# Kernel optimization log

Measured on AMD Instinct MI355X. Metric: run time of the kernel, lower is better.

## Reference

```python
import jax, jax.numpy as jnp
import numpy as np

ROPE_BASE = 10000.0
NEG_INF = -1e30

def _apply_rope(x):
    # x: [B, H, T, D]; interleaved-pair RoPE (torchtune style), positions along axis -2.
    B, H, T, D = x.shape
    inv_freq = 1.0 / (ROPE_BASE ** (jnp.arange(0, D, 2, dtype=jnp.float32) / D))  # [D/2]
    ang = jnp.arange(T, dtype=jnp.float32)[:, None] * inv_freq[None, :]           # [T, D/2]
    cos, sin = jnp.cos(ang), jnp.sin(ang)
    x1, x2 = x[..., 0::2], x[..., 1::2]                                           # [B,H,T,D/2]
    rot = jnp.stack([x1 * cos - x2 * sin, x1 * sin + x2 * cos], axis=-1)          # [B,H,T,D/2,2]
    return rot.reshape(B, H, T, D).astype(x.dtype)

def setup_inputs() -> dict:
    key = jax.random.key(0)
    ks = jax.random.split(key, 5)
    B, T, C = 2, 2048, 1024
    s = 1.0 / np.sqrt(C)
    return {
        "x":  jax.random.normal(ks[0], (B, T, C), jnp.float32),
        "Wq": jax.random.normal(ks[1], (C, C), jnp.float32) * s,
        "bq": jnp.zeros((C,), jnp.float32),
        "Wk": jax.random.normal(ks[2], (C, C), jnp.float32) * s,
        "bk": jnp.zeros((C,), jnp.float32),
        "Wv": jax.random.normal(ks[3], (C, C), jnp.float32) * s,
        "bv": jnp.zeros((C,), jnp.float32),
        "Wo": jax.random.normal(ks[4], (C, C), jnp.float32) * s,
        "bo": jnp.zeros((C,), jnp.float32),
    }

def reference(x, Wq, bq, Wk, bk, Wv, bv, Wo, bo):
    B, T, C = x.shape
    H = 16
    D = C // H
    # QKV projections (torch Linear: x @ W.T + b), split heads -> [B, H, T, D]
    def proj(W, b):
        return (jnp.einsum('btc,oc->bto', x, W) + b).reshape(B, T, H, D).transpose(0, 2, 1, 3)
    q = _apply_rope(proj(Wq, bq))
    k = _apply_rope(proj(Wk, bk))
    v = proj(Wv, bv)
    # Causal scaled dot-product attention
    scale = 1.0 / jnp.sqrt(jnp.asarray(D, x.dtype))
    scores = jnp.einsum('bhqd,bhkd->bhqk', q, k) * scale                          # [B,H,T,T]
    causal = jnp.tril(jnp.ones((T, T), dtype=bool))
    scores = jnp.where(causal, scores, NEG_INF)
    probs = jax.nn.softmax(scores, axis=-1)
    y = jnp.einsum('bhqk,bhkd->bhqd', probs, v)                                   # [B,H,T,D]
    y = y.transpose(0, 2, 1, 3).reshape(B, T, C)
    # Output projection (dropout is identity in eval mode)
    return jnp.einsum('btc,oc->bto', y, Wo) + bo
```

## Files before the change

kernel.cpp:

```cpp
#include <hip/hip_runtime.h>

#define BB 2
#define TT 2048
#define CC 1024
#define HH 16
#define DD 64
#define KDIM 1024
#define MROWS (BB*TT)

typedef __attribute__((ext_vector_type(8))) short  frag_b16;
typedef __attribute__((ext_vector_type(4))) float  f32x4;
typedef __attribute__((ext_vector_type(4))) unsigned short us4;
typedef __attribute__((ext_vector_type(8))) unsigned short us8;
typedef __attribute__((ext_vector_type(4))) _Float16 f16x4;
typedef __attribute__((ext_vector_type(8))) _Float16 f16x8;

__device__ __forceinline__ unsigned short f2bf(float f) {
    unsigned int u = __builtin_bit_cast(unsigned int, f);
    u += 0x7FFFu + ((u >> 16) & 1u);
    return (unsigned short)(u >> 16);
}

__device__ __forceinline__ void gl_lds16(const void* g, void* l) {
    __builtin_amdgcn_global_load_lds(
        (const __attribute__((address_space(1))) unsigned int*)g,
        (__attribute__((address_space(3))) unsigned int*)l, 16, 0, 0);
}

__global__ __launch_bounds__(256) void cvt_all(
        const float* __restrict__ x,  const float* __restrict__ w0,
        const float* __restrict__ w1, const float* __restrict__ w2,
        const float* __restrict__ w3, unsigned short* __restrict__ dst) {
    const size_t NX = (size_t)MROWS * CC;
    const size_t NW = (size_t)CC * CC;
    size_t i = ((size_t)blockIdx.x * 256 + threadIdx.x) * 4;
    const float* src; size_t off;
    if (i < NX) { src = x; off = i; }
    else {
        size_t j = i - NX;
        int t = (int)(j >> 20);
        src = (t == 0) ? w0 : (t == 1) ? w1 : (t == 2) ? w2 : w3;
        off = j & (NW - 1);
    }
    float4 f = *reinterpret_cast<const float4*>(src + off);
    us4 o;
    o.x = f2bf(f.x); o.y = f2bf(f.y); o.z = f2bf(f.z); o.w = f2bf(f.w);
    *reinterpret_cast<us4*>(dst + i) = o;
}

__global__ __launch_bounds__(256, 3) void qkv_gemm_rope(
        const unsigned short* __restrict__ X,
        const unsigned short* __restrict__ Wq,
        const unsigned short* __restrict__ Wk,
        const unsigned short* __restrict__ Wv,
        const float* __restrict__ bq, const float* __restrict__ bk,
        const float* __restrict__ bv,
        unsigned short* __restrict__ Qo,
        unsigned short* __restrict__ Ko,
        _Float16* __restrict__ VTo)
{
    const int z = blockIdx.z;
    const unsigned short* W = (z == 0) ? Wq : (z == 1) ? Wk : Wv;
    const float* bias = (z == 0) ? bq : (z == 1) ? bk : bv;

    const int tid = threadIdx.x;
    const int wave = tid >> 6;
    const int lane = tid & 63;
    const int l16 = lane & 15;
    const int quad = lane >> 4;

    const int bx = blockIdx.x * 128;
    const int by = blockIdx.y * 128;
    const int row0 = bx + (wave >> 1) * 64;
    const int col0 = by + (wave & 1) * 64;

    __shared__ __align__(16) char smem[36864];
    unsigned short (*Xa)[32] = (unsigned short(*)[32])smem;
    unsigned short (*Wb)[32] = (unsigned short(*)[32])(smem + 8192);
    _Float16 (*Vl)[64][72] = (_Float16(*)[64][72])smem;

    f32x4 acc[4][4] = {};

    const int c0 = tid, c1 = tid + 256;
    const int r0s = c0 >> 2, o0s = (c0 & 3) * 8;
    const int r1s = c1 >> 2, o1s = (c1 & 3) * 8;

    for (int kk = 0; kk < KDIM; kk += 32) {
        gl_lds16(X + (size_t)(bx + r0s) * KDIM + kk + o0s, (unsigned short*)Xa + c0 * 8);
        gl_lds16(X + (size_t)(bx + r1s) * KDIM + kk + o1s, (unsigned short*)Xa + c1 * 8);
        gl_lds16(W + (size_t)(by + r0s) * KDIM + kk + o0s, (unsigned short*)Wb + c0 * 8);
        gl_lds16(W + (size_t)(by + r1s) * KDIM + kk + o1s, (unsigned short*)Wb + c1 * 8);
        __syncthreads();

        frag_b16 a[4], b[4];
#pragma unroll
        for (int r = 0; r < 4; ++r)
            a[r] = *reinterpret_cast<const frag_b16*>(
                &Xa[(wave >> 1) * 64 + r * 16 + l16][quad * 8]);
#pragma unroll
        for (int c = 0; c < 4; ++c)
            b[c] = *reinterpret_cast<const frag_b16*>(
                &Wb[(wave & 1) * 64 + c * 16 + l16][quad * 8]);
#pragma unroll
        for (int r = 0; r < 4; ++r)
#pragma unroll
            for (int c = 0; c < 4; ++c)
                acc[r][c] = __builtin_amdgcn_mfma_f32_16x16x32_bf16(a[r], b[c], acc[r][c], 0, 0, 0);
        __syncthreads();
    }

    if (z == 2) {
#pragma unroll
        for (int r = 0; r < 4; ++r)
#pragma unroll
            for (int c = 0; c < 4; ++c) {
                f16x4 pk;
#pragma unroll
                for (int g = 0; g < 4; ++g)
                    pk[g] = (_Float16)(acc[r][c][g] + bias[col0 + c * 16 + l16]);
                *reinterpret_cast<f16x4*>(&Vl[wave][c * 16 + l16][r * 16 + quad * 4]) = pk;
            }
        const int b_ = row0 >> 11;
        const int t_base = row0 & (TT - 1);
        const int h = col0 >> 6;
        const int dl = lane >> 3;
        const int t8 = (lane & 7) * 8;
        __builtin_amdgcn_s_waitcnt(0);
#pragma unroll
        for (int i = 0; i < 8; ++i) {
            int d = i * 8 + dl;
            f16x8 v = *reinterpret_cast<const f16x8*>(&Vl[wave][d][t8]);
            *reinterpret_cast<f16x8*>(
                &VTo[((size_t)(b_ * HH + h) * DD + d) * TT + t_base + t8]) = v;
        }
    } else {
        const float qscale = (z == 0) ? 0.125f : 1.0f;
#pragma unroll
        for (int r = 0; r < 4; ++r)
#pragma unroll
            for (int c = 0; c < 4; ++c)
#pragma unroll
                for (int g = 0; g < 4; ++g) {
                    int n = row0 + r * 16 + quad * 4 + g;
                    int o = col0 + c * 16 + l16;
                    float v = acc[r][c][g] + bias[o];
                    int b_ = n >> 11;
                    int t  = n & (TT - 1);
                    int h  = o >> 6;
                    int d  = o & (DD - 1);
                    float pv = __shfl_xor(v, 1);
                    float inv = __expf(-(float)(d & ~1) * (9.210340371976184f / (float)DD));
                    float ang = (float)t * inv;
                    float sn, cs;
                    __sincosf(ang, &sn, &cs);
                    float outv = (d & 1) ? (pv * sn + v * cs) : (v * cs - pv * sn);
                    unsigned short* dst = (z == 0) ? Qo : Ko;
                    dst[((size_t)(b_ * HH + h) * TT + t) * DD + d] = f2bf(outv * qscale);
                }
    }
}

__global__ __launch_bounds__(256, 2) void attn(
        const unsigned short* __restrict__ Q,
        const unsigned short* __restrict__ K,
        const _Float16* __restrict__ VT,
        unsigned short* __restrict__ Y)
{
    const int pair = blockIdx.x;
    const int bh = blockIdx.y;
    const int tid = threadIdx.x;
    const int w = tid >> 6;
    const int lane = tid & 63;
    const int l16 = lane & 15;
    const int quad = lane >> 4;

    const unsigned short* Qp = Q + (size_t)bh * TT * DD;
    const unsigned short* Kp = K + (size_t)bh * TT * DD;
    const _Float16* Vp = VT + (size_t)bh * DD * TT;

    __shared__ unsigned short Kl[2][64][64];
    __shared__ _Float16 Vl[2][64][64];
    __shared__ unsigned short Ylds[4][16][72];

    const int ca = tid, cb = tid + 256;
    const int ra = ca >> 3, oa = ((ca & 7) ^ (ra & 7)) * 8;
    const int rb = cb >> 3, ob = ((cb & 7) ^ (rb & 7)) * 8;
    const int sw = (l16 & 7);

    const int b_ = bh >> 4, h = bh & (HH - 1);

#pragma unroll 1
    for (int seg = 0; seg < 2; ++seg) {
        const int qblk = seg ? (31 - pair) : pair;
        const int q0 = qblk * 64;
        const int q = q0 + w * 16 + l16;

        frag_b16 bq[2];
#pragma unroll
        for (int dk = 0; dk < 2; ++dk)
            bq[dk] = *reinterpret_cast<const frag_b16*>(
                Qp + (size_t)q * DD + dk * 32 + quad * 8);

        f32x4 yacc[4] = {};
        float m = -INFINITY, l = 0.f;

        const int ntiles = qblk + 1;

        gl_lds16(Kp + (size_t)ra * DD + oa, (unsigned short*)&Kl[0][0][0] + ca * 8);
        gl_lds16(Kp + (size_t)rb * DD + ob, (unsigned short*)&Kl[0][0][0] + cb * 8);
        gl_lds16(Vp + (size_t)ra * TT + oa, (_Float16*)&Vl[0][0][0] + ca * 8);
        gl_lds16(Vp + (size_t)rb * TT + ob, (_Float16*)&Vl[0][0][0] + cb * 8);

#pragma unroll 1
        for (int it = 0; it < ntiles; ++it) {
            __syncthreads();
            const int bsel = it & 1;
            if (it + 1 < ntiles) {
                const int jn = (it + 1) * 64;
                const int bn = bsel ^ 1;
                gl_lds16(Kp + (size_t)(jn + ra) * DD + oa, (unsigned short*)&Kl[bn][0][0] + ca * 8);
                gl_lds16(Kp + (size_t)(jn + rb) * DD + ob, (unsigned short*)&Kl[bn][0][0] + cb * 8);
                gl_lds16(Vp + (size_t)ra * TT + jn + oa, (_Float16*)&Vl[bn][0][0] + ca * 8);
                gl_lds16(Vp + (size_t)rb * TT + jn + ob, (_Float16*)&Vl[bn][0][0] + cb * 8);
            }
            const int j0 = it * 64;

            f32x4 s[4];
#pragma unroll
            for (int mt = 0; mt < 4; ++mt) {
                frag_b16 ak0 = *reinterpret_cast<const frag_b16*>(
                    &Kl[bsel][mt * 16 + l16][(quad ^ sw) * 8]);
                frag_b16 ak1 = *reinterpret_cast<const frag_b16*>(
                    &Kl[bsel][mt * 16 + l16][((4 + quad) ^ sw) * 8]);
                f32x4 t = {};
                t = __builtin_amdgcn_mfma_f32_16x16x32_bf16(ak0, bq[0], t, 0, 0, 0);
                t = __builtin_amdgcn_mfma_f32_16x16x32_bf16(ak1, bq[1], t, 0, 0, 0);
                s[mt] = t;
            }

            float nm = -INFINITY;
            if (it == qblk) {
#pragma unroll
                for (int mt = 0; mt < 4; ++mt)
#pragma unroll
                    for (int g = 0; g < 4; ++g) {
                        int key = j0 + mt * 16 + quad * 4 + g;
                        float v = s[mt][g];
                        if (key > q) v = -1e30f;
                        s[mt][g] = v;
                        nm = fmaxf(nm, v);
                    }
            } else {
#pragma unroll
                for (int mt = 0; mt < 4; ++mt)
#pragma unroll
                    for (int g = 0; g < 4; ++g)
                        nm = fmaxf(nm, s[mt][g]);
            }
            nm = fmaxf(nm, __shfl_xor(nm, 16));
            nm = fmaxf(nm, __shfl_xor(nm, 32));

            float mn = fmaxf(m, nm);
            float alpha = __expf(m - mn);
            m = mn;

            float rs = 0.f;
#pragma unroll
            for (int mt = 0; mt < 4; ++mt)
#pragma unroll
                for (int g = 0; g < 4; ++g) {
                    float e = __expf(s[mt][g] - m);
                    s[mt][g] = e;
                    rs += e;
                }
            rs += __shfl_xor(rs, 16);
            rs += __shfl_xor(rs, 32);
            l = l * alpha + rs;

            f16x4 pb[4];
#pragma unroll
            for (int kt = 0; kt < 4; ++kt)
#pragma unroll
                for (int g = 0; g < 4; ++g)
                    pb[kt][g] = (_Float16)s[kt][g];

#pragma unroll
            for (int dt = 0; dt < 4; ++dt) {
                f32x4 ya = yacc[dt];
#pragma unroll
                for (int g = 0; g < 4; ++g) ya[g] *= alpha;
#pragma unroll
                for (int kt = 0; kt < 4; ++kt) {
                    int colp = (kt * 2 + (quad >> 1)) ^ sw;
                    f16x4 av = *reinterpret_cast<const f16x4*>(
                        &Vl[bsel][dt * 16 + l16][colp * 8 + (quad & 1) * 4]);
                    ya = __builtin_amdgcn_mfma_f32_16x16x16f16(av, pb[kt], ya, 0, 0, 0);
                }
                yacc[dt] = ya;
            }
        }

        __syncthreads();

        float rl = 1.f / l;
#pragma unroll
        for (int dt = 0; dt < 4; ++dt)
#pragma unroll
            for (int g = 0; g < 4; ++g)
                Ylds[w][l16][dt * 16 + quad * 4 + g] = f2bf(yacc[dt][g] * rl);

#pragma unroll
        for (int i = 0; i < 2; ++i) {
            int idx = i * 64 + lane;
            int r = idx >> 3, c8 = (idx & 7) * 8;
            us8 v = *reinterpret_cast<const us8*>(&Ylds[w][r][c8]);
            *reinterpret_cast<us8*>(
                &Y[(size_t)(b_ * TT + q0 + w * 16 + r) * CC + h * DD + c8]) = v;
        }
    }
}

__global__ __launch_bounds__(256, 2) void out_gemm(
        const unsigned short* __restrict__ Y,
        const unsigned short* __restrict__ Wo,
        const float* __restrict__ bo,
        float* __restrict__ out)
{
    const int tid = threadIdx.x;
    const int wave = tid >> 6;
    const int lane = tid & 63;
    const int l16 = lane & 15;
    const int quad = lane >> 4;

    const int bx = blockIdx.x * 128;
    const int by = blockIdx.y * 128;
    const int row0 = bx + (wave >> 1) * 64;
    const int col0 = by + (wave & 1) * 64;

    __shared__ unsigned short Xa[128][32];
    __shared__ unsigned short Wb[128][32];

    f32x4 acc[4][4] = {};

    const int c0 = tid, c1 = tid + 256;
    const int r0s = c0 >> 2, o0s = (c0 & 3) * 8;
    const int r1s = c1 >> 2, o1s = (c1 & 3) * 8;

    for (int kk = 0; kk < KDIM; kk += 32) {
        gl_lds16(Y  + (size_t)(bx + r0s) * KDIM + kk + o0s, (unsigned short*)Xa + c0 * 8);
        gl_lds16(Y  + (size_t)(bx + r1s) * KDIM + kk + o1s, (unsigned short*)Xa + c1 * 8);
        gl_lds16(Wo + (size_t)(by + r0s) * KDIM + kk + o0s, (unsigned short*)Wb + c0 * 8);
        gl_lds16(Wo + (size_t)(by + r1s) * KDIM + kk + o1s, (unsigned short*)Wb + c1 * 8);
        __syncthreads();

        frag_b16 a[4], b[4];
#pragma unroll
        for (int r = 0; r < 4; ++r)
            a[r] = *reinterpret_cast<const frag_b16*>(
                &Xa[(wave >> 1) * 64 + r * 16 + l16][quad * 8]);
#pragma unroll
        for (int c = 0; c < 4; ++c)
            b[c] = *reinterpret_cast<const frag_b16*>(
                &Wb[(wave & 1) * 64 + c * 16 + l16][quad * 8]);
#pragma unroll
        for (int r = 0; r < 4; ++r)
#pragma unroll
            for (int c = 0; c < 4; ++c)
                acc[r][c] = __builtin_amdgcn_mfma_f32_16x16x32_bf16(a[r], b[c], acc[r][c], 0, 0, 0);
        __syncthreads();
    }

#pragma unroll
    for (int r = 0; r < 4; ++r)
#pragma unroll
        for (int c = 0; c < 4; ++c)
#pragma unroll
            for (int g = 0; g < 4; ++g) {
                int n = row0 + r * 16 + quad * 4 + g;
                int o = col0 + c * 16 + l16;
                out[(size_t)n * CC + o] = acc[r][c][g] + bo[o];
            }
}

extern "C" void kernel_launch(void* const* d_in, const int* in_sizes, int n_in,
                              void* d_out, int out_size, void* d_ws, size_t ws_size,
                              hipStream_t stream) {
    const float* x  = (const float*)d_in[0];
    const float* Wq = (const float*)d_in[1];
    const float* bq = (const float*)d_in[2];
    const float* Wk = (const float*)d_in[3];
    const float* bk = (const float*)d_in[4];
    const float* Wv = (const float*)d_in[5];
    const float* bv = (const float*)d_in[6];
    const float* Wo = (const float*)d_in[7];
    const float* bo = (const float*)d_in[8];
    float* out = (float*)d_out;

    unsigned short* ws = (unsigned short*)d_ws;
    const size_t NX = (size_t)MROWS * CC;
    const size_t NW = (size_t)CC * CC;
    unsigned short* xb  = ws;
    unsigned short* wqb = xb  + NX;
    unsigned short* wkb = wqb + NW;
    unsigned short* wvb = wkb + NW;
    unsigned short* wob = wvb + NW;
    unsigned short* Qr  = wob + NW;
    unsigned short* Kr  = Qr  + NX;
    _Float16*       VTb = (_Float16*)(Kr + NX);
    unsigned short* Yb  = (unsigned short*)(VTb + NX);

    const size_t NALL = NX + 4 * NW;
    cvt_all<<<dim3((unsigned)(NALL / 1024)), 256, 0, stream>>>(x, Wq, Wk, Wv, Wo, xb);

    qkv_gemm_rope<<<dim3(MROWS / 128, CC / 128, 3), 256, 0, stream>>>(
        xb, wqb, wkb, wvb, bq, bk, bv, Qr, Kr, VTb);

    attn<<<dim3(16, BB * HH), 256, 0, stream>>>(Qr, Kr, VTb, Yb);

    out_gemm<<<dim3(MROWS / 128, CC / 128), 256, 0, stream>>>(Yb, wob, bo, out);
}
```

Measured before the change: 190.0 us.

## Widen attention key tiles, use exp2 softmax, and compute RoPE incrementally

The attention kernel now processes 128-key tiles per iteration instead of 64, which halves the number of barrier and softmax steps. It folds log2(e) into the Q scale so exp2 can be used, and remaps the 1D grid so blocks are ordered by batch-head. The QKV epilogue replaces per-element sincos with a rotation recurrence built from a few sincos calls per column. The wider tiles raise LDS use and register pressure. The V-tile swizzle only XORs with the row's low 3 bits across 16 chunks, and the recurrence slightly changes RoPE numerics.

Result: faster. 183.5 us (-3.4%).

```diff
diff --git a/kernel.cpp b/kernel.cpp
--- a/kernel.cpp
+++ b/kernel.cpp
@@ -14,6 +14,8 @@
 typedef __attribute__((ext_vector_type(8))) unsigned short us8;
 typedef __attribute__((ext_vector_type(4))) _Float16 f16x4;
 typedef __attribute__((ext_vector_type(8))) _Float16 f16x8;
+
+#define EXP2F(x) __builtin_amdgcn_exp2f(x)
 
 __device__ __forceinline__ unsigned short f2bf(float f) {
     unsigned int u = __builtin_bit_cast(unsigned int, f);
@@ -134,29 +136,40 @@
                 &VTo[((size_t)(b_ * HH + h) * DD + d) * TT + t_base + t8]) = v;
         }
     } else {
-        const float qscale = (z == 0) ? 0.125f : 1.0f;
-#pragma unroll
-        for (int r = 0; r < 4; ++r)
-#pragma unroll
-            for (int c = 0; c < 4; ++c)
+        const float qsc = (z == 0) ? 0.180336888f : 1.0f;
+        unsigned short* dst = (z == 0) ? Qo : Ko;
+        const int b_ = row0 >> 11;
+        const int tq0 = (row0 & (TT - 1)) + quad * 4;
+#pragma unroll
+        for (int c = 0; c < 4; ++c) {
+            const int o = col0 + c * 16 + l16;
+            const int h = o >> 6, d = o & (DD - 1);
+            const float inv = __expf(-(float)(d & ~1) * (9.210340371976184f / (float)DD));
+            float cs0, sn0, cs1, sn1, cs16, sn16;
+            __sincosf((float)tq0 * inv, &sn0, &cs0);
+            __sincosf(inv, &sn1, &cs1);
+            __sincosf(16.f * inv, &sn16, &cs16);
+            float cr = cs0, sr = sn0;
+#pragma unroll
+            for (int r = 0; r < 4; ++r) {
+                float cg = cr, sg = sr;
 #pragma unroll
                 for (int g = 0; g < 4; ++g) {
                     int n = row0 + r * 16 + quad * 4 + g;
-                    int o = col0 + c * 16 + l16;
+                    int t = n & (TT - 1);
                     float v = acc[r][c][g] + bias[o];
-                    int b_ = n >> 11;
-                    int t  = n & (TT - 1);
-                    int h  = o >> 6;
-                    int d  = o & (DD - 1);
                     float pv = __shfl_xor(v, 1);
-                    float inv = __expf(-(float)(d & ~1) * (9.210340371976184f / (float)DD));
-                    float ang = (float)t * inv;
-                    float sn, cs;
-                    __sincosf(ang, &sn, &cs);
-                    float outv = (d & 1) ? (pv * sn + v * cs) : (v * cs - pv * sn);
-                    unsigned short* dst = (z == 0) ? Qo : Ko;
-                    dst[((size_t)(b_ * HH + h) * TT + t) * DD + d] = f2bf(outv * qscale);
+                    float outv = (d & 1) ? (pv * sg + v * cg) : (v * cg - pv * sg);
+                    dst[((size_t)(b_ * HH + h) * TT + t) * DD + d] = f2bf(outv * qsc);
+                    float cn = cg * cs1 - sg * sn1;
+                    sg = sg * cs1 + cg * sn1;
+                    cg = cn;
                 }
+                float crn = cr * cs16 - sr * sn16;
+                sr = sr * cs16 + cr * sn16;
+                cr = crn;
+            }
+        }
     }
 }
 
@@ -166,8 +179,9 @@
         const _Float16* __restrict__ VT,
         unsigned short* __restrict__ Y)
 {
-    const int pair = blockIdx.x;
-    const int bh = blockIdx.y;
+    const int b1d = blockIdx.x;
+    const int bh = (b1d & 7) * 4 + ((b1d >> 3) & 3);
+    const int pair = b1d >> 5;
     const int tid = threadIdx.x;
     const int w = tid >> 6;
     const int lane = tid & 63;
@@ -178,15 +192,11 @@
     const unsigned short* Kp = K + (size_t)bh * TT * DD;
     const _Float16* Vp = VT + (size_t)bh * DD * TT;
 
-    __shared__ unsigned short Kl[2][64][64];
-    __shared__ _Float16 Vl[2][64][64];
+    __shared__ unsigned short Kl[2][128][64];
+    __shared__ _Float16 Vl[2][64][128];
     __shared__ unsigned short Ylds[4][16][72];
 
-    const int ca = tid, cb = tid + 256;
-    const int ra = ca >> 3, oa = ((ca & 7) ^ (ra & 7)) * 8;
-    const int rb = cb >> 3, ob = ((cb & 7) ^ (rb & 7)) * 8;
     const int sw = (l16 & 7);
-
     const int b_ = bh >> 4, h = bh & (HH - 1);
 
 #pragma unroll 1
@@ -204,30 +214,40 @@
         f32x4 yacc[4] = {};
         float m = -INFINITY, l = 0.f;
 
-        const int ntiles = qblk + 1;
-
-        gl_lds16(Kp + (size_t)ra * DD + oa, (unsigned short*)&Kl[0][0][0] + ca * 8);
-        gl_lds16(Kp + (size_t)rb * DD + ob, (unsigned short*)&Kl[0][0][0] + cb * 8);
-        gl_lds16(Vp + (size_t)ra * TT + oa, (_Float16*)&Vl[0][0][0] + ca * 8);
-        gl_lds16(Vp + (size_t)rb * TT + ob, (_Float16*)&Vl[0][0][0] + cb * 8);
+        const int ntiles = (qblk >> 1) + 1;
+
+#pragma unroll
+        for (int i = 0; i < 4; ++i) {
+            int n = tid + 256 * i;
+            int kr = n >> 3,  kc = ((n & 7)  ^ (kr & 7)) * 8;
+            int vr = n >> 4,  vc = ((n & 15) ^ (vr & 7)) * 8;
+            gl_lds16(Kp + (size_t)kr * DD + kc, (unsigned short*)&Kl[0][0][0] + n * 8);
+            gl_lds16(Vp + (size_t)vr * TT + vc, (_Float16*)&Vl[0][0][0] + n * 8);
+        }
 
 #pragma unroll 1
         for (int it = 0; it < ntiles; ++it) {
             __syncthreads();
             const int bsel = it & 1;
             if (it + 1 < ntiles) {
-                const int jn = (it + 1) * 64;
+                const int jn = (it + 1) * 128;
                 const int bn = bsel ^ 1;
-                gl_lds16(Kp + (size_t)(jn + ra) * DD + oa, (unsigned short*)&Kl[bn][0][0] + ca * 8);
-                gl_lds16(Kp + (size_t)(jn + rb) * DD + ob, (unsigned short*)&Kl[bn][0][0] + cb * 8);
-                gl_lds16(Vp + (size_t)ra * TT + jn + oa, (_Float16*)&Vl[bn][0][0] + ca * 8);
-                gl_lds16(Vp + (size_t)rb * TT + jn + ob, (_Float16*)&Vl[bn][0][0] + cb * 8);
-            }
-            const int j0 = it * 64;
-
-            f32x4 s[4];
-#pragma unroll
-            for (int mt = 0; mt < 4; ++mt) {
+#pragma unroll
+                for (int i = 0; i < 4; ++i) {
+                    int n = tid + 256 * i;
+                    int kr = n >> 3,  kc = ((n & 7)  ^ (kr & 7)) * 8;
+                    int vr = n >> 4,  vc = ((n & 15) ^ (vr & 7)) * 8;
+                    gl_lds16(Kp + (size_t)(jn + kr) * DD + kc,
+                             (unsigned short*)&Kl[bn][0][0] + n * 8);
+                    gl_lds16(Vp + (size_t)vr * TT + jn + vc,
+                             (_Float16*)&Vl[bn][0][0] + n * 8);
+                }
+            }
+            const int j0 = it * 128;
+
+            f32x4 s[8];
+#pragma unroll
+            for (int mt = 0; mt < 8; ++mt) {
                 frag_b16 ak0 = *reinterpret_cast<const frag_b16*>(
                     &Kl[bsel][mt * 16 + l16][(quad ^ sw) * 8]);
                 frag_b16 ak1 = *reinterpret_cast<const frag_b16*>(
@@ -239,9 +259,9 @@
             }
 
             float nm = -INFINITY;
-            if (it == qblk) {
-#pragma unroll
-                for (int mt = 0; mt < 4; ++mt)
+            if (it == ntiles - 1) {
+#pragma unroll
+                for (int mt = 0; mt < 8; ++mt)
 #pragma unroll
                     for (int g = 0; g < 4; ++g) {
                         int key = j0 + mt * 16 + quad * 4 + g;
@@ -252,7 +272,7 @@
                     }
             } else {
 #pragma unroll
-                for (int mt = 0; mt < 4; ++mt)
+                for (int mt = 0; mt < 8; ++mt)
 #pragma unroll
                     for (int g = 0; g < 4; ++g)
                         nm = fmaxf(nm, s[mt][g]);
@@ -261,36 +281,30 @@
             nm = fmaxf(nm, __shfl_xor(nm, 32));
 
             float mn = fmaxf(m, nm);
-            float alpha = __expf(m - mn);
+            float alpha = EXP2F(m - mn);
             m = mn;
 
             float rs = 0.f;
-#pragma unroll
-            for (int mt = 0; mt < 4; ++mt)
+            f16x4 pb[8];
+#pragma unroll
+            for (int mt = 0; mt < 8; ++mt)
 #pragma unroll
                 for (int g = 0; g < 4; ++g) {
-                    float e = __expf(s[mt][g] - m);
-                    s[mt][g] = e;
+                    float e = EXP2F(s[mt][g] - m);
+                    pb[mt][g] = (_Float16)e;
                     rs += e;
                 }
             rs += __shfl_xor(rs, 16);
             rs += __shfl_xor(rs, 32);
             l = l * alpha + rs;
 
-            f16x4 pb[4];
-#pragma unroll
-            for (int kt = 0; kt < 4; ++kt)
-#pragma unroll
-                for (int g = 0; g < 4; ++g)
-                    pb[kt][g] = (_Float16)s[kt][g];
-
 #pragma unroll
             for (int dt = 0; dt < 4; ++dt) {
                 f32x4 ya = yacc[dt];
 #pragma unroll
                 for (int g = 0; g < 4; ++g) ya[g] *= alpha;
 #pragma unroll
-                for (int kt = 0; kt < 4; ++kt) {
+                for (int kt = 0; kt < 8; ++kt) {
                     int colp = (kt * 2 + (quad >> 1)) ^ sw;
                     f16x4 av = *reinterpret_cast<const f16x4*>(
                         &Vl[bsel][dt * 16 + l16][colp * 8 + (quad & 1) * 4]);
@@ -415,7 +429,7 @@
     qkv_gemm_rope<<<dim3(MROWS / 128, CC / 128, 3), 256, 0, stream>>>(
         xb, wqb, wkb, wvb, bq, bk, bv, Qr, Kr, VTb);
 
-    attn<<<dim3(16, BB * HH), 256, 0, stream>>>(Qr, Kr, VTb, Yb);
+    attn<<<dim3(512), 256, 0, stream>>>(Qr, Kr, VTb, Yb);
 
     out_gemm<<<dim3(MROWS / 128, CC / 128), 256, 0, stream>>>(Yb, wob, bo, out);
 }
```
